# Performance work log

Hardware: AMD Instinct MI355X
Metric: run time of the kernel (lower is better)

The kernel has to match this reference:

```python
import jax, jax.numpy as jnp
import numpy as np

GRID_SIZE = 8
MARGIN = 1.0
NUM_NEG = 4
SOS_NEG = 8
LOSS_LAMBDA = 1.0
IMG_H, IMG_W = 960, 1280  # desc2 is the stride-GRID_SIZE feature map of this image
BIG = 5.0    # fill for radius-masked entries in FOS distance matrix (> max unit-desc dist 2)
HUGE = 1e6   # fill for invalid entries in SOS candidate scores


def _l2n(x, eps=1e-8):
    return x / (jnp.linalg.norm(x, axis=-1, keepdims=True) + eps)


def _pdist(a, b, eps=1e-12):
    # a: B x N x C, b: B x M x C -> B x N x M euclidean distances
    sq = (jnp.sum(a * a, -1)[..., :, None] + jnp.sum(b * b, -1)[..., None, :]
          - 2.0 * jnp.einsum('bnc,bmc->bnm', a, b))
    return jnp.sqrt(jnp.maximum(sq, eps))


def _bilinear(desc, pts):
    # desc: B x C x H x W, pts: B x N x 2 in (y, x) image-pixel coords -> B x N x C
    B, C, H, W = desc.shape
    g = pts / GRID_SIZE - 0.5  # image coords -> feature-grid coords
    gy = jnp.clip(g[..., 0], 0.0, H - 1.0)
    gx = jnp.clip(g[..., 1], 0.0, W - 1.0)
    y0 = jnp.clip(jnp.floor(gy).astype(jnp.int32), 0, H - 2)
    x0 = jnp.clip(jnp.floor(gx).astype(jnp.int32), 0, W - 2)
    wy = (gy - y0)[:, None, :]
    wx = (gx - x0)[:, None, :]
    flat = desc.reshape(B, C, H * W)
    gat = lambda yi, xi: jnp.take_along_axis(flat, (yi * W + xi)[:, None, :], axis=2)
    v00, v01 = gat(y0, x0), gat(y0, x0 + 1)
    v10, v11 = gat(y0 + 1, x0), gat(y0 + 1, x0 + 1)
    out = (v00 * (1 - wy) * (1 - wx) + v01 * (1 - wy) * wx
           + v10 * wy * (1 - wx) + v11 * wy * wx)
    return out.transpose(0, 2, 1)


def _forward(kp1, w_kp1, kp1_desc, desc2, homo12):
    r = 2.0 * GRID_SIZE  # spatial masking radius
    d1 = _l2n(kp1_desc)                       # B x N x C
    w_desc = _l2n(_bilinear(desc2, w_kp1))    # B x N x C interpolated warped descriptors

    # visibility of kp1 under homography homo12 (kp stored as (y, x))
    ones = jnp.ones_like(kp1[..., :1])
    p = jnp.concatenate([kp1[..., 1:2], kp1[..., 0:1], ones], -1)  # (x, y, 1)
    q = jnp.einsum('bij,bnj->bni', homo12, p)
    qx = q[..., 0] / (q[..., 2] + 1e-8)
    qy = q[..., 1] / (q[..., 2] + 1e-8)
    vis = ((qx >= 0) & (qx < IMG_W) & (qy >= 0) & (qy < IMG_H)).astype(d1.dtype)
    denom = jnp.sum(vis) + 1e-8

    # ---- FOS: hard quad triplet with radius masking ----
    pos = jnp.sqrt(jnp.sum((d1 - w_desc) ** 2, -1) + 1e-12)  # B x N
    D = _pdist(d1, w_desc)          # B x N x N cross descriptor distances
    s22 = _pdist(w_kp1, w_kp1)      # B x N x N warped-coordinate distances
    Dm = jnp.where(s22 <= r, BIG, D)  # mask spatial near-positives (incl. diagonal)
    neg1 = -jax.lax.top_k(-Dm, NUM_NEG)[0]                       # hardest negs per row anchor
    neg2 = -jax.lax.top_k(-Dm.transpose(0, 2, 1), NUM_NEG)[0]    # per column anchor
    t1 = jnp.mean(jax.nn.relu(MARGIN + pos[..., None] - neg1), -1)
    t2 = jnp.mean(jax.nn.relu(MARGIN + pos[..., None] - neg2), -1)
    fos = jnp.sum(vis * 0.5 * (t1 + t2)) / denom

    # ---- SOS: radius-masked second-order similarity regularizer ----
    s11 = _pdist(kp1, kp1)
    d11 = _pdist(d1, d1)
    d22 = _pdist(w_desc, w_desc)
    valid = (s11 > r) & (s22 > r)
    score = jnp.where(valid, d11, HUGE)
    nscore, idx = jax.lax.top_k(-score, SOS_NEG)  # sos_neg hardest valid neighbors
    sel_d11 = -nscore
    sel_d22 = jnp.take_along_axis(d22, idx, axis=2)
    diff2 = jnp.where(sel_d11 < HUGE * 0.1, (sel_d11 - sel_d22) ** 2, 0.0)
    sos_i = jnp.sqrt(jnp.sum(diff2, -1) + 1e-12)
    sos = jnp.sum(vis * sos_i) / denom

    return (fos + sos) * LOSS_LAMBDA


def setup_inputs() -> dict:
    key = jax.random.key(0)
    k1, k2, k3, k4, k5 = jax.random.split(key, 5)
    B, N, C, H, W = 2, 4096, 128, 120, 160
    scale = jnp.array([IMG_H - 1.0, IMG_W - 1.0], dtype=jnp.float32)
    kp1 = jax.random.uniform(k1, (B, N, 2), dtype=jnp.float32) * scale
    w_kp1 = jax.random.uniform(k2, (B, N, 2), dtype=jnp.float32) * scale
    kp1_desc = jax.random.normal(k3, (B, N, C), dtype=jnp.float32)
    desc2 = jax.random.normal(k4, (B, C, H, W), dtype=jnp.float32)
    homo12 = (jnp.tile(jnp.eye(3, dtype=jnp.float32), (B, 1, 1))
              + 0.001 * jax.random.normal(k5, (B, 3, 3), dtype=jnp.float32))
    return {'kp1': kp1, 'w_kp1': w_kp1, 'kp1_desc': kp1_desc,
            'desc2': desc2, 'homo12': homo12}


def reference(kp1, w_kp1, kp1_desc, desc2, homo12):
    return _forward(kp1, w_kp1, kp1_desc, desc2, homo12)
```

## Files before the change

### kernel.cpp

```cpp
#include <hip/hip_runtime.h>
#include <hip/hip_fp16.h>
#include <math.h>

#define NPTS 4096
#define CDIM 128
#define FH 120
#define FW 160
#define PIX (FH * FW)

typedef __attribute__((ext_vector_type(8))) short short8_t;
typedef __attribute__((ext_vector_type(4))) float float4_t;
typedef __attribute__((ext_vector_type(2))) unsigned short ushort2_t;

#define OFF_FRAG  0
#define OFF_WDB   1048576
#define OFF_JA    1572864
#define OFF_JB    1605632
#define OFF_POS   1622016
#define OFF_VIS   1630208
#define OFF_ACC   1638400
#define OFF_D2T   2031632
#define OFF_PARTS 2031632
#define OFF_END   4489232

__device__ __forceinline__ unsigned short f2bf(float f) {
  unsigned int u = __float_as_uint(f);
  u = (u + 0x7fffu + ((u >> 16) & 1u)) >> 16;
  return (unsigned short)u;
}

__device__ __forceinline__ float wavesum(float v) {
#pragma unroll
  for (int off = 1; off < 64; off <<= 1) v += __shfl_xor(v, off, 64);
  return v;
}

typedef const __attribute__((address_space(1))) unsigned int gu32_t;
typedef __attribute__((address_space(3))) unsigned int lu32_t;
__device__ __forceinline__ void gl_lds16(const void* g, void* l) {
  __builtin_amdgcn_global_load_lds((gu32_t*)g, (lu32_t*)l, 16, 0, 0);
}

__global__ __launch_bounds__(256) void transpose_desc2(
    const float* __restrict__ d2, unsigned short* __restrict__ out) {
  __shared__ unsigned short tile[64][130];
  const int bp = blockIdx.x;
  const int b = bp / 300;
  const int p0 = (bp - b * 300) * 64;
  const int tid = threadIdx.x;
  const int grp = tid >> 6, lp = tid & 63;
#pragma unroll 4
  for (int r = 0; r < 32; ++r) {
    int c = (r << 2) | grp;
    float v = d2[((size_t)b * CDIM + c) * PIX + p0 + lp];
    tile[lp][c] = __half_as_ushort(__float2half(v));
  }
  __syncthreads();
  unsigned int* ob = (unsigned int*)(out + ((size_t)b * PIX + p0) * CDIM);
#pragma unroll
  for (int i = 0; i < 16; ++i) {
    int u = (i << 8) | tid;
    int p = u >> 6, cc = (u & 63) << 1;
    unsigned int lo = tile[p][cc], hi = tile[p][cc + 1];
    ob[u] = lo | (hi << 16);
  }
}

#define PREP_TAIL() do {                                                        \
  {                                                                             \
    const int T = (p & (NPTS - 1)) >> 4, cRow = p & 15;                         \
    const int kcL = lane >> 4, quadL = (lane >> 2) & 3, jjL = (lane & 3) * 2;   \
    const size_t off = (size_t)(quadL * 16 + cRow) * 8 + jjL;                   \
    const size_t tb = (((size_t)b * 256 + T) * 2) * 4;                          \
    ushort2_t st; st.x = f2bf(d0); st.y = f2bf(d1v);                            \
    ushort2_t sw; sw.x = f2bf(e0); sw.y = f2bf(e1);                             \
    *(ushort2_t*)(frag + (tb + kcL) * 512 + off) = st;                          \
    *(ushort2_t*)(frag + (tb + 4 + kcL) * 512 + off) = sw;                      \
    ushort2_t swr; swr.x = f2bf(e0); swr.y = f2bf(e1);                          \
    *(ushort2_t*)(wdb + (size_t)p * CDIM + c2) = swr;                           \
  }                                                                             \
  float dd0 = d0 - e0, dd1 = d1v - e1;                                          \
  float ssp = wavesum(dd0 * dd0 + dd1 * dd1);                                   \
  if (lane == 0) {                                                              \
    pos[p] = sqrtf(ssp + 1e-12f);                                               \
    float ky = kp1[p * 2 + 0], kx = kp1[p * 2 + 1];                             \
    jA[p] = make_float4(ky, kx, y, x);                                          \
    jb1[p] = -0.5f * n1;                                                        \
    jb2[p] = -0.5f * n2;                                                        \
    const float* h = homo + b * 9;                                              \
    float t0 = h[0] * kx + h[1] * ky + h[2];                                    \
    float t1 = h[3] * kx + h[4] * ky + h[5];                                    \
    float t2 = h[6] * kx + h[7] * ky + h[8];                                    \
    float qx = t0 / (t2 + 1e-8f), qy = t1 / (t2 + 1e-8f);                       \
    vis[p] = (qx >= 0.0f && qx < 1280.0f && qy >= 0.0f && qy < 960.0f)          \
                 ? 1.0f : 0.0f;                                                 \
  }                                                                             \
} while (0)

__global__ __launch_bounds__(256) void prep_t(
    const float* __restrict__ kp1, const float* __restrict__ wkp1,
    const float* __restrict__ desc, const unsigned short* __restrict__ d2t,
    const float* __restrict__ homo,
    unsigned short* __restrict__ frag, unsigned short* __restrict__ wdb,
    float4* __restrict__ jA, float* __restrict__ jb1, float* __restrict__ jb2,
    float* __restrict__ pos, float* __restrict__ vis, float* __restrict__ acc) {
  const int tid = threadIdx.x;
  if (blockIdx.x == 0 && tid < 4) acc[tid] = 0.0f;
  const int p = blockIdx.x * 4 + (tid >> 6);
  const int lane = tid & 63;
  const int b = p >> 12;
  const int c2 = lane * 2;

  float2 v = *(const float2*)(desc + (size_t)p * CDIM + c2);
  float ss = wavesum(v.x * v.x + v.y * v.y);
  float inv = 1.0f / (sqrtf(ss) + 1e-8f);
  float d0 = v.x * inv, d1v = v.y * inv;
  float n1 = ss * inv * inv;

  float y = wkp1[p * 2 + 0], x = wkp1[p * 2 + 1];
  float gy = fminf(fmaxf(y * 0.125f - 0.5f, 0.0f), (float)(FH - 1));
  float gx = fminf(fmaxf(x * 0.125f - 0.5f, 0.0f), (float)(FW - 1));
  int y0 = (int)floorf(gy); y0 = min(max(y0, 0), FH - 2);
  int x0 = (int)floorf(gx); x0 = min(max(x0, 0), FW - 2);
  float wy = gy - (float)y0, wx = gx - (float)x0;
  float w00 = (1 - wy) * (1 - wx), w01 = (1 - wy) * wx;
  float w10 = wy * (1 - wx), w11 = wy * wx;
  const unsigned int* t00 = (const unsigned int*)
      (d2t + ((size_t)b * PIX + y0 * FW + x0) * CDIM) + lane;
  unsigned int u00 = t00[0], u01 = t00[64];
  unsigned int u10 = t00[FW * 64], u11 = t00[FW * 64 + 64];
  float2 f00 = __half22float2(*(const __half2*)&u00);
  float2 f01 = __half22float2(*(const __half2*)&u01);
  float2 f10 = __half22float2(*(const __half2*)&u10);
  float2 f11 = __half22float2(*(const __half2*)&u11);
  float wv0 = f00.x * w00 + f01.x * w01 + f10.x * w10 + f11.x * w11;
  float wv1 = f00.y * w00 + f01.y * w01 + f10.y * w10 + f11.y * w11;
  float ss2 = wavesum(wv0 * wv0 + wv1 * wv1);
  float inv2 = 1.0f / (sqrtf(ss2) + 1e-8f);
  float e0 = wv0 * inv2, e1 = wv1 * inv2;
  float n2 = ss2 * inv2 * inv2;

  PREP_TAIL();
}

__global__ __launch_bounds__(256) void prep_g(
    const float* __restrict__ kp1, const float* __restrict__ wkp1,
    const float* __restrict__ desc, const float* __restrict__ desc2,
    const float* __restrict__ homo,
    unsigned short* __restrict__ frag, unsigned short* __restrict__ wdb,
    float4* __restrict__ jA, float* __restrict__ jb1, float* __restrict__ jb2,
    float* __restrict__ pos, float* __restrict__ vis, float* __restrict__ acc) {
  const int tid = threadIdx.x;
  if (blockIdx.x == 0 && tid < 4) acc[tid] = 0.0f;
  const int p = blockIdx.x * 4 + (tid >> 6);
  const int lane = tid & 63;
  const int b = p >> 12;
  const int c2 = lane * 2;

  float2 v = *(const float2*)(desc + (size_t)p * CDIM + c2);
  float ss = wavesum(v.x * v.x + v.y * v.y);
  float inv = 1.0f / (sqrtf(ss) + 1e-8f);
  float d0 = v.x * inv, d1v = v.y * inv;
  float n1 = ss * inv * inv;

  float y = wkp1[p * 2 + 0], x = wkp1[p * 2 + 1];
  float gy = fminf(fmaxf(y * 0.125f - 0.5f, 0.0f), (float)(FH - 1));
  float gx = fminf(fmaxf(x * 0.125f - 0.5f, 0.0f), (float)(FW - 1));
  int y0 = (int)floorf(gy); y0 = min(max(y0, 0), FH - 2);
  int x0 = (int)floorf(gx); x0 = min(max(x0, 0), FW - 2);
  float wy = gy - (float)y0, wx = gx - (float)x0;
  float w00 = (1 - wy) * (1 - wx), w01 = (1 - wy) * wx;
  float w10 = wy * (1 - wx), w11 = wy * wx;
  const float* q0 = desc2 + ((size_t)b * CDIM + c2) * PIX + y0 * FW + x0;
  const float* q1 = q0 + PIX;
  float wv0 = q0[0] * w00 + q0[1] * w01 + q0[FW] * w10 + q0[FW + 1] * w11;
  float wv1 = q1[0] * w00 + q1[1] * w01 + q1[FW] * w10 + q1[FW + 1] * w11;
  float ss2 = wavesum(wv0 * wv0 + wv1 * wv1);
  float inv2 = 1.0f / (sqrtf(ss2) + 1e-8f);
  float e0 = wv0 * inv2, e1 = wv1 * inv2;
  float n2 = ss2 * inv2 * inv2;

  PREP_TAIL();
}

__device__ __forceinline__ void ins4m(float v, float* L) {
  float p0 = L[0]; L[0] = fmaxf(L[0], v);
  float p1 = L[1]; L[1] = __builtin_amdgcn_fmed3f(p0, L[1], v);
  float p2 = L[2]; L[2] = __builtin_amdgcn_fmed3f(p1, L[2], v);
  L[3] = __builtin_amdgcn_fmed3f(p2, L[3], v);
}
__device__ __forceinline__ void ins6m(float v, float* L) {
  float p0 = L[0]; L[0] = fmaxf(L[0], v);
  float p1 = L[1]; L[1] = __builtin_amdgcn_fmed3f(p0, L[1], v);
  float p2 = L[2]; L[2] = __builtin_amdgcn_fmed3f(p1, L[2], v);
  float p3 = L[3]; L[3] = __builtin_amdgcn_fmed3f(p2, L[3], v);
  float p4 = L[4]; L[4] = __builtin_amdgcn_fmed3f(p3, L[4], v);
  L[5] = __builtin_amdgcn_fmed3f(p4, L[5], v);
}
__device__ __forceinline__ void ins10m(float v, float* L) {
  float p0 = L[0]; L[0] = fmaxf(L[0], v);
  float pk = p0;
#pragma unroll
  for (int k = 1; k < 9; ++k) {
    float cur = L[k];
    L[k] = __builtin_amdgcn_fmed3f(pk, cur, v);
    pk = cur;
  }
  L[9] = __builtin_amdgcn_fmed3f(pk, L[9], v);
}

__device__ __forceinline__ float packkey(float s, int j) {
  return __uint_as_float((__float_as_uint(s) & 0xFFFFF000u) | (unsigned)j);
}

#define TILE_ONE(BP, J0, M1, M2) do {                                           \
  short8_t Ad[4], Aw[4];                                                        \
  _Pragma("unroll")                                                             \
  for (int kc = 0; kc < 4; ++kc) {                                              \
    Ad[kc] = *(const short8_t*)((BP) + kc * 512 + lane * 8);                    \
    Aw[kc] = *(const short8_t*)((BP) + (4 + kc) * 512 + lane * 8);              \
  }                                                                             \
  float4_t aD, aDt, a11;                                                        \
  aD[0] = (M2).x; aD[1] = (M2).y; aD[2] = (M2).z; aD[3] = (M2).w;               \
  aDt[0] = (M1).x; aDt[1] = (M1).y; aDt[2] = (M1).z; aDt[3] = (M1).w;           \
  a11 = aDt;                                                                    \
  __builtin_amdgcn_s_setprio(1);                                                \
  _Pragma("unroll")                                                             \
  for (int kc = 0; kc < 4; ++kc) {                                              \
    aD  = __builtin_amdgcn_mfma_f32_16x16x32_bf16(Aw[kc], Bd[kc], aD,  0,0,0);  \
    aDt = __builtin_amdgcn_mfma_f32_16x16x32_bf16(Ad[kc], Bw[kc], aDt, 0,0,0);  \
    a11 = __builtin_amdgcn_mfma_f32_16x16x32_bf16(Ad[kc], Bd[kc], a11, 0,0,0);  \
  }                                                                             \
  __builtin_amdgcn_s_setprio(0);                                                \
  _Pragma("unroll")                                                             \
  for (int reg = 0; reg < 4; ++reg) {                                           \
    const int jj = (J0) + (quad << 2) + reg;                                    \
    ins4m(packkey(aD[reg], jj), fD);                                            \
    ins4m(packkey(aDt[reg], jj), fDt);                                          \
    ins6m(packkey(a11[reg], jj), fS);                                           \
  }                                                                             \
} while (0)

#define STAGE_T(BI, TG) do {                                                    \
  gl_lds16((TG) + ch * 512 + lane * 8, &buf[BI][ch * 512]);                     \
  gl_lds16((TG) + (ch + 1) * 512 + lane * 8, &buf[BI][(ch + 1) * 512]);         \
} while (0)

__global__ __launch_bounds__(256, 4) void loss_main(
    const unsigned short* __restrict__ frag,
    const float* __restrict__ jb1g, const float* __restrict__ jb2g,
    float* __restrict__ parts) {
  __shared__ __align__(16) unsigned short buf[4][4096];

  const int tid = threadIdx.x;
  const int bid = blockIdx.x;
  const int combo = ((bid & 7) << 1) | (bid >> 9);
  const int b   = combo >> 3;
  const int seg = combo & 7;
  const int g   = (bid >> 3) & 63;
  const int wave = tid >> 6, lane = tid & 63;
  const int quad = lane >> 4;
  const int base = b * NPTS;
  const int jbase = seg << 9;

  short8_t Bd[4], Bw[4];
  {
    const unsigned short* fb =
        frag + (((size_t)b * 256 + (g * 4 + wave)) * 8) * 512 + (size_t)lane * 8;
#pragma unroll
    for (int kc = 0; kc < 4; ++kc) {
      Bd[kc] = *(const short8_t*)(fb + kc * 512);
      Bw[kc] = *(const short8_t*)(fb + (4 + kc) * 512);
    }
  }

  float fD[4], fDt[4], fS[6];
#pragma unroll
  for (int k = 0; k < 4; ++k) { fD[k] = -1e30f; fDt[k] = -1e30f; }
#pragma unroll
  for (int k = 0; k < 6; ++k) fS[k] = -1e30f;

  const unsigned short* fa = frag + (((size_t)b * 256 + (jbase >> 4)) * 8) * 512;
  const float* j1b = jb1g + base;
  const float* j2b = jb2g + base;
  const int ch = wave << 1;

  STAGE_T(0, fa);
  STAGE_T(1, fa + 4096);
  float4 m1c = *(const float4*)(j1b + jbase + (quad << 2));
  float4 m2c = *(const float4*)(j2b + jbase + (quad << 2));

  for (int t = 0; t < 30; ++t) {
    STAGE_T((t + 2) & 3, fa + (size_t)(t + 2) * 4096);
    const int jn = jbase + ((t + 1) << 4) + (quad << 2);
    float4 m1n = *(const float4*)(j1b + jn);
    float4 m2n = *(const float4*)(j2b + jn);
    asm volatile("s_waitcnt vmcnt(4)" ::: "memory");
    __builtin_amdgcn_s_barrier();
    asm volatile("" ::: "memory");
    TILE_ONE(&buf[t & 3][0], jbase + (t << 4), m1c, m2c);
    m1c = m1n; m2c = m2n;
  }
  {
    const int jn = jbase + (31 << 4) + (quad << 2);
    float4 m1n = *(const float4*)(j1b + jn);
    float4 m2n = *(const float4*)(j2b + jn);
    asm volatile("s_waitcnt vmcnt(2)" ::: "memory");
    __builtin_amdgcn_s_barrier();
    asm volatile("" ::: "memory");
    TILE_ONE(&buf[30 & 3][0], jbase + (30 << 4), m1c, m2c);
    m1c = m1n; m2c = m2n;
  }
  {
    asm volatile("s_waitcnt vmcnt(0)" ::: "memory");
    __builtin_amdgcn_s_barrier();
    asm volatile("" ::: "memory");
    TILE_ONE(&buf[31 & 3][0], jbase + (31 << 4), m1c, m2c);
  }

  float eD[6], eDt[6], eS[10];
#pragma unroll
  for (int k = 0; k < 4; ++k) { eD[k] = fD[k]; eDt[k] = fDt[k]; }
  eD[4] = eD[5] = eDt[4] = eDt[5] = -1e30f;
#pragma unroll
  for (int k = 0; k < 6; ++k) eS[k] = fS[k];
  eS[6] = eS[7] = eS[8] = eS[9] = -1e30f;

  {
    float tmp[10];
#pragma unroll
    for (int off = 16; off <= 32; off <<= 1) {
#pragma unroll
      for (int k = 0; k < 6; ++k) tmp[k] = eD[k];
#pragma unroll
      for (int k = 0; k < 6; ++k) ins6m(__shfl_xor(tmp[k], off, 64), eD);
#pragma unroll
      for (int k = 0; k < 6; ++k) tmp[k] = eDt[k];
#pragma unroll
      for (int k = 0; k < 6; ++k) ins6m(__shfl_xor(tmp[k], off, 64), eDt);
#pragma unroll
      for (int k = 0; k < 10; ++k) tmp[k] = eS[k];
#pragma unroll
      for (int k = 0; k < 10; ++k) ins10m(__shfl_xor(tmp[k], off, 64), eS);
    }
  }

  if (lane < 16) {
    float* P = parts + (size_t)(seg * 22) * 8192 +
               (base + g * 64 + wave * 16 + lane);
#pragma unroll
    for (int k = 0; k < 6; ++k) {
      P[(size_t)k * 8192] = eD[k];
      P[(size_t)(6 + k) * 8192] = eDt[k];
    }
#pragma unroll
    for (int k = 0; k < 10; ++k) P[(size_t)(12 + k) * 8192] = eS[k];
  }
}

__device__ __forceinline__ float bflo(unsigned int u) { return __uint_as_float(u << 16); }
__device__ __forceinline__ float bfhi(unsigned int u) { return __uint_as_float(u & 0xFFFF0000u); }

__global__ __launch_bounds__(256) void merge_filter(
    const float* __restrict__ parts, const float4* __restrict__ jAg,
    const float* __restrict__ jb1g, const float* __restrict__ jb2g,
    const float* __restrict__ posg,
    const float* __restrict__ visg, const unsigned short* __restrict__ wdb,
    float* __restrict__ accum, float* __restrict__ out) {
  __shared__ int sJ[256];
  __shared__ float sD11[256], sD22[256], sT[64], sVis[32], sN2[32];
  const int tid = threadIdx.x;
  const int a0 = blockIdx.x * 32;

  if (tid < 64) {
    const int al = tid & 31;
    const int type = tid >> 5;
    const int a = a0 + al;
    const int base = a & ~(NPTS - 1);
    float L[6];
#pragma unroll
    for (int k = 0; k < 6; ++k) L[k] = -1e30f;
    const float* P = parts + (size_t)(type * 6) * 8192 + a;
#pragma unroll
    for (int s = 0; s < 8; ++s) {
#pragma unroll
      for (int k = 0; k < 6; ++k) ins6m(P[(size_t)(s * 22 + k) * 8192], L);
    }
    const float4 own = jAg[a];
    const float pv = posg[a];
    const float nsel = -2.0f * (type ? jb2g[a] : jb1g[a]);
    float ts = 0.0f;
    int got = 0;
#pragma unroll
    for (int k = 0; k < 6; ++k) {
      int j = (int)(__float_as_uint(L[k]) & 0xFFFu);
      float4 jc = jAg[base + j];
      float dz = own.z - jc.z, dw = own.w - jc.w;
      if (got < 4 && dz * dz + dw * dw > 256.0f) {
        float d2 = fmaf(-2.0f, L[k], nsel);
        ts += fmaxf(1.0f + pv - sqrtf(fmaxf(d2, 1e-12f)), 0.0f);
        got++;
      }
    }
    sT[tid] = ts;
  } else if (tid < 96) {
    const int al = tid - 64;
    const int a = a0 + al;
    const int base = a & ~(NPTS - 1);
    float S[10];
#pragma unroll
    for (int k = 0; k < 10; ++k) S[k] = -1e30f;
    const float* P = parts + (size_t)12 * 8192 + a;
#pragma unroll
    for (int s = 0; s < 8; ++s) {
#pragma unroll
      for (int k = 0; k < 10; ++k) ins10m(P[(size_t)(s * 22 + k) * 8192], S);
    }
    const float4 own = jAg[a];
    const float n1i = -2.0f * jb1g[a];
    int m = 0;
#pragma unroll
    for (int k = 0; k < 10; ++k) {
      int j = (int)(__float_as_uint(S[k]) & 0xFFFu);
      float4 jc = jAg[base + j];
      float ay = own.x - jc.x, ax = own.y - jc.y;
      float wz = own.z - jc.z, ww = own.w - jc.w;
      if (m < 8 && ay * ay + ax * ax > 256.0f && wz * wz + ww * ww > 256.0f) {
        sJ[al * 8 + m] = base + j;
        sD11[al * 8 + m] = sqrtf(fmaxf(fmaf(-2.0f, S[k], n1i), 1e-12f));
        m++;
      }
    }
    for (int k = m; k < 8; ++k) sJ[al * 8 + k] = -1;
    sVis[al] = visg[a];
    sN2[al] = -2.0f * jb2g[a];
  }
  __syncthreads();

  {
    const int slot = tid;
    const int al = slot >> 3;
    const int j = sJ[slot];
    float d22 = 0.0f;
    if (j >= 0) {
      const uint4* pi = (const uint4*)(wdb + (size_t)(a0 + al) * CDIM);
      const uint4* pj = (const uint4*)(wdb + (size_t)j * CDIM);
      float dot = 0.0f;
#pragma unroll
      for (int qq = 0; qq < 16; ++qq) {
        uint4 ui = pi[qq], uj = pj[qq];
        dot = fmaf(bflo(ui.x), bflo(uj.x), dot); dot = fmaf(bfhi(ui.x), bfhi(uj.x), dot);
        dot = fmaf(bflo(ui.y), bflo(uj.y), dot); dot = fmaf(bfhi(ui.y), bfhi(uj.y), dot);
        dot = fmaf(bflo(ui.z), bflo(uj.z), dot); dot = fmaf(bfhi(ui.z), bfhi(uj.z), dot);
        dot = fmaf(bflo(ui.w), bflo(uj.w), dot); dot = fmaf(bfhi(ui.w), bfhi(uj.w), dot);
      }
      d22 = sqrtf(fmaxf(fmaf(-2.0f, jb2g[j] + dot, sN2[al]), 1e-12f));
    }
    sD22[slot] = d22;
  }
  __syncthreads();

  float contrib = 0.0f, vsum = 0.0f;
  if (tid < 32) {
    float s = 0.0f;
#pragma unroll
    for (int k = 0; k < 8; ++k) {
      if (sJ[tid * 8 + k] >= 0) {
        float d = sD11[tid * 8 + k] - sD22[tid * 8 + k];
        s = fmaf(d, d, s);
      }
    }
    contrib = sVis[tid] * (0.125f * (sT[tid] + sT[32 + tid]) + sqrtf(s + 1e-12f));
    vsum = sVis[tid];
  }
  if (tid < 64) {
#pragma unroll
    for (int off = 32; off >= 1; off >>= 1) {
      contrib += __shfl_down(contrib, off, 64);
      vsum += __shfl_down(vsum, off, 64);
    }
    if (tid == 0) {
      atomicAdd(&accum[0], contrib);
      atomicAdd(&accum[1], vsum);
      __threadfence();
      float old = atomicAdd(&accum[2], 1.0f);
      if (old == 255.0f) {
        float t = atomicAdd(&accum[0], 0.0f);
        float v = atomicAdd(&accum[1], 0.0f);
        out[0] = t / (v + 1e-8f);
      }
    }
  }
}

extern "C" void kernel_launch(void* const* d_in, const int* in_sizes, int n_in,
                              void* d_out, int out_size, void* d_ws, size_t ws_size,
                              hipStream_t stream) {
  (void)in_sizes; (void)n_in; (void)out_size;
  const float* kp1   = (const float*)d_in[0];
  const float* wkp1  = (const float*)d_in[1];
  const float* desc  = (const float*)d_in[2];
  const float* desc2 = (const float*)d_in[3];
  const float* homo  = (const float*)d_in[4];
  float* ws = (float*)d_ws;
  unsigned short* frag = (unsigned short*)(ws + OFF_FRAG);
  unsigned short* wdb  = (unsigned short*)(ws + OFF_WDB);
  float4* jA = (float4*)(ws + OFF_JA);
  float* jb1 = ws + OFF_JB;
  float* jb2 = ws + OFF_JB + 8192;
  float* pos = ws + OFF_POS;
  float* vis = ws + OFF_VIS;
  float* acc = ws + OFF_ACC;
  float* parts = ws + OFF_PARTS;
  unsigned short* d2t = (unsigned short*)(ws + OFF_D2T);

  if (ws_size >= (size_t)OFF_END * 4) {
    transpose_desc2<<<600, 256, 0, stream>>>(desc2, d2t);
    prep_t<<<2048, 256, 0, stream>>>(kp1, wkp1, desc, d2t, homo,
                                     frag, wdb, jA, jb1, jb2, pos, vis, acc);
  } else {
    prep_g<<<2048, 256, 0, stream>>>(kp1, wkp1, desc, desc2, homo,
                                     frag, wdb, jA, jb1, jb2, pos, vis, acc);
  }
  loss_main<<<1024, 256, 0, stream>>>(frag, jb1, jb2, parts);
  merge_filter<<<256, 256, 0, stream>>>(parts, jA, jb1, jb2, pos, vis, wdb, acc,
                                        (float*)d_out);
}
```

Baseline: 149.6 us.

## Switch pairwise distance kernel to 32x32x16 MFMA tiles with larger chunks

Reorganizes the bf16 fragment layout into 32-point tiles and moves the main all-pairs kernel from 16x16x32 to 32x32x16 MFMA, so each wave holds a 32-row B fragment and processes 32-column chunks staged through a 4-deep LDS pipeline. The jb norms are preloaded into LDS, the grid is halved to 512 blocks with lower occupancy, and top-k per lane widens (6/6/8 instead of 4/4/6) with only one cross-half shuffle merge. The aim is fewer MFMA issues, fewer reloads of the A chunks and a cheaper reduction, at the cost of more registers, larger partial-result buffers and more insertion work in merge_filter.

```diff
diff --git a/kernel.cpp b/kernel.cpp
--- a/kernel.cpp
+++ b/kernel.cpp
@@ -10,6 +10,7 @@
 
 typedef __attribute__((ext_vector_type(8))) short short8_t;
 typedef __attribute__((ext_vector_type(4))) float float4_t;
+typedef __attribute__((ext_vector_type(16))) float f32x16_t;
 typedef __attribute__((ext_vector_type(2))) unsigned short ushort2_t;
 
 #define OFF_FRAG  0
@@ -68,14 +69,15 @@
 
 #define PREP_TAIL() do {                                                        \
   {                                                                             \
-    const int T = (p & (NPTS - 1)) >> 4, cRow = p & 15;                         \
-    const int kcL = lane >> 4, quadL = (lane >> 2) & 3, jjL = (lane & 3) * 2;   \
-    const size_t off = (size_t)(quadL * 16 + cRow) * 8 + jjL;                   \
-    const size_t tb = (((size_t)b * 256 + T) * 2) * 4;                          \
+    const int pc = p & (NPTS - 1);                                              \
+    const int Tc = pc >> 5, m = pc & 31;                                        \
+    const int kq = lane >> 3, hi2 = (lane >> 2) & 1, j0 = (lane & 3) * 2;       \
+    const size_t off = (size_t)kq * 512 + (m + 32 * hi2) * 8 + j0;              \
+    const size_t cb = ((size_t)b * 128 + Tc) * 8192;                            \
     ushort2_t st; st.x = f2bf(d0); st.y = f2bf(d1v);                            \
     ushort2_t sw; sw.x = f2bf(e0); sw.y = f2bf(e1);                             \
-    *(ushort2_t*)(frag + (tb + kcL) * 512 + off) = st;                          \
-    *(ushort2_t*)(frag + (tb + 4 + kcL) * 512 + off) = sw;                      \
+    *(ushort2_t*)(frag + cb + off) = st;                                        \
+    *(ushort2_t*)(frag + cb + 4096 + off) = sw;                                 \
     ushort2_t swr; swr.x = f2bf(e0); swr.y = f2bf(e1);                          \
     *(ushort2_t*)(wdb + (size_t)p * CDIM + c2) = swr;                           \
   }                                                                             \
@@ -183,12 +185,6 @@
   PREP_TAIL();
 }
 
-__device__ __forceinline__ void ins4m(float v, float* L) {
-  float p0 = L[0]; L[0] = fmaxf(L[0], v);
-  float p1 = L[1]; L[1] = __builtin_amdgcn_fmed3f(p0, L[1], v);
-  float p2 = L[2]; L[2] = __builtin_amdgcn_fmed3f(p1, L[2], v);
-  L[3] = __builtin_amdgcn_fmed3f(p2, L[3], v);
-}
 __device__ __forceinline__ void ins6m(float v, float* L) {
   float p0 = L[0]; L[0] = fmaxf(L[0], v);
   float p1 = L[1]; L[1] = __builtin_amdgcn_fmed3f(p0, L[1], v);
@@ -197,164 +193,172 @@
   float p4 = L[4]; L[4] = __builtin_amdgcn_fmed3f(p3, L[4], v);
   L[5] = __builtin_amdgcn_fmed3f(p4, L[5], v);
 }
-__device__ __forceinline__ void ins10m(float v, float* L) {
+__device__ __forceinline__ void ins8m(float v, float* L) {
   float p0 = L[0]; L[0] = fmaxf(L[0], v);
   float pk = p0;
 #pragma unroll
-  for (int k = 1; k < 9; ++k) {
+  for (int k = 1; k < 7; ++k) {
     float cur = L[k];
     L[k] = __builtin_amdgcn_fmed3f(pk, cur, v);
     pk = cur;
   }
-  L[9] = __builtin_amdgcn_fmed3f(pk, L[9], v);
+  L[7] = __builtin_amdgcn_fmed3f(pk, L[7], v);
+}
+__device__ __forceinline__ void ins12m(float v, float* L) {
+  float p0 = L[0]; L[0] = fmaxf(L[0], v);
+  float pk = p0;
+#pragma unroll
+  for (int k = 1; k < 11; ++k) {
+    float cur = L[k];
+    L[k] = __builtin_amdgcn_fmed3f(pk, cur, v);
+    pk = cur;
+  }
+  L[11] = __builtin_amdgcn_fmed3f(pk, L[11], v);
 }
 
 __device__ __forceinline__ float packkey(float s, int j) {
   return __uint_as_float((__float_as_uint(s) & 0xFFFFF000u) | (unsigned)j);
 }
 
-#define TILE_ONE(BP, J0, M1, M2) do {                                           \
-  short8_t Ad[4], Aw[4];                                                        \
+#define CHUNK(T) do {                                                           \
+  const unsigned short* bp = &buf[(T) & 3][0];                                  \
+  float4 m1v[4], m2v[4];                                                        \
   _Pragma("unroll")                                                             \
-  for (int kc = 0; kc < 4; ++kc) {                                              \
-    Ad[kc] = *(const short8_t*)((BP) + kc * 512 + lane * 8);                    \
-    Aw[kc] = *(const short8_t*)((BP) + (4 + kc) * 512 + lane * 8);              \
+  for (int q = 0; q < 4; ++q) {                                                 \
+    m1v[q] = *(const float4*)&jbL[(T) * 32 + q * 8 + hi * 4];                   \
+    m2v[q] = *(const float4*)&jbL[512 + (T) * 32 + q * 8 + hi * 4];             \
   }                                                                             \
-  float4_t aD, aDt, a11;                                                        \
-  aD[0] = (M2).x; aD[1] = (M2).y; aD[2] = (M2).z; aD[3] = (M2).w;               \
-  aDt[0] = (M1).x; aDt[1] = (M1).y; aDt[2] = (M1).z; aDt[3] = (M1).w;           \
-  a11 = aDt;                                                                    \
+  f32x16_t aD, aDt, a11;                                                        \
+  _Pragma("unroll")                                                             \
+  for (int q = 0; q < 4; ++q) {                                                 \
+    _Pragma("unroll")                                                           \
+    for (int i = 0; i < 4; ++i) {                                               \
+      aD[q * 4 + i] = m2v[q][i];                                                \
+      aDt[q * 4 + i] = m1v[q][i];                                               \
+      a11[q * 4 + i] = m1v[q][i];                                               \
+    }                                                                           \
+  }                                                                             \
   __builtin_amdgcn_s_setprio(1);                                                \
   _Pragma("unroll")                                                             \
-  for (int kc = 0; kc < 4; ++kc) {                                              \
-    aD  = __builtin_amdgcn_mfma_f32_16x16x32_bf16(Aw[kc], Bd[kc], aD,  0,0,0);  \
-    aDt = __builtin_amdgcn_mfma_f32_16x16x32_bf16(Ad[kc], Bw[kc], aDt, 0,0,0);  \
-    a11 = __builtin_amdgcn_mfma_f32_16x16x32_bf16(Ad[kc], Bd[kc], a11, 0,0,0);  \
+  for (int kq = 0; kq < 8; ++kq) {                                              \
+    short8_t Ad = *(const short8_t*)(bp + kq * 512 + lane * 8);                 \
+    short8_t Aw = *(const short8_t*)(bp + 4096 + kq * 512 + lane * 8);          \
+    aD  = __builtin_amdgcn_mfma_f32_32x32x16_bf16(Aw, Bd[kq], aD,  0, 0, 0);    \
+    aDt = __builtin_amdgcn_mfma_f32_32x32x16_bf16(Ad, Bw[kq], aDt, 0, 0, 0);    \
+    a11 = __builtin_amdgcn_mfma_f32_32x32x16_bf16(Ad, Bd[kq], a11, 0, 0, 0);    \
   }                                                                             \
   __builtin_amdgcn_s_setprio(0);                                                \
+  const int jjp = jbase + (T) * 32 + (hi << 2);                                 \
   _Pragma("unroll")                                                             \
-  for (int reg = 0; reg < 4; ++reg) {                                           \
-    const int jj = (J0) + (quad << 2) + reg;                                    \
-    ins4m(packkey(aD[reg], jj), fD);                                            \
-    ins4m(packkey(aDt[reg], jj), fDt);                                          \
-    ins6m(packkey(a11[reg], jj), fS);                                           \
+  for (int reg = 0; reg < 16; ++reg) {                                          \
+    const int jj = jjp | ((reg & 3) | ((reg >> 2) << 3));                       \
+    ins6m(packkey(aD[reg], jj), fD);                                            \
+    ins6m(packkey(aDt[reg], jj), fDt);                                          \
+    ins8m(packkey(a11[reg], jj), fS);                                           \
   }                                                                             \
 } while (0)
 
-#define STAGE_T(BI, TG) do {                                                    \
-  gl_lds16((TG) + ch * 512 + lane * 8, &buf[BI][ch * 512]);                     \
-  gl_lds16((TG) + (ch + 1) * 512 + lane * 8, &buf[BI][(ch + 1) * 512]);         \
+#define STAGE_C(BI, CT) do {                                                    \
+  const unsigned short* gsrc =                                                  \
+      fa + (size_t)(CT) * 8192 + wave * 512 + lane * 8;                         \
+  _Pragma("unroll")                                                             \
+  for (int i = 0; i < 4; ++i)                                                   \
+    gl_lds16(gsrc + i * 2048, &buf[BI][i * 2048 + wave * 512]);                 \
 } while (0)
 
-__global__ __launch_bounds__(256, 4) void loss_main(
+__global__ __launch_bounds__(256, 2) void loss_main(
     const unsigned short* __restrict__ frag,
     const float* __restrict__ jb1g, const float* __restrict__ jb2g,
     float* __restrict__ parts) {
-  __shared__ __align__(16) unsigned short buf[4][4096];
+  __shared__ __align__(16) unsigned short buf[4][8192];
+  __shared__ __align__(16) float jbL[1024];
 
   const int tid = threadIdx.x;
   const int bid = blockIdx.x;
-  const int combo = ((bid & 7) << 1) | (bid >> 9);
+  const int combo = ((bid & 7) << 1) | (bid >> 8);
   const int b   = combo >> 3;
   const int seg = combo & 7;
-  const int g   = (bid >> 3) & 63;
+  const int g   = (bid >> 3) & 31;
   const int wave = tid >> 6, lane = tid & 63;
-  const int quad = lane >> 4;
+  const int hi = lane >> 5;
   const int base = b * NPTS;
   const int jbase = seg << 9;
 
-  short8_t Bd[4], Bw[4];
+  short8_t Bd[8], Bw[8];
   {
     const unsigned short* fb =
-        frag + (((size_t)b * 256 + (g * 4 + wave)) * 8) * 512 + (size_t)lane * 8;
-#pragma unroll
-    for (int kc = 0; kc < 4; ++kc) {
-      Bd[kc] = *(const short8_t*)(fb + kc * 512);
-      Bw[kc] = *(const short8_t*)(fb + (4 + kc) * 512);
-    }
-  }
-
-  float fD[4], fDt[4], fS[6];
-#pragma unroll
-  for (int k = 0; k < 4; ++k) { fD[k] = -1e30f; fDt[k] = -1e30f; }
-#pragma unroll
-  for (int k = 0; k < 6; ++k) fS[k] = -1e30f;
-
-  const unsigned short* fa = frag + (((size_t)b * 256 + (jbase >> 4)) * 8) * 512;
-  const float* j1b = jb1g + base;
-  const float* j2b = jb2g + base;
-  const int ch = wave << 1;
-
-  STAGE_T(0, fa);
-  STAGE_T(1, fa + 4096);
-  float4 m1c = *(const float4*)(j1b + jbase + (quad << 2));
-  float4 m2c = *(const float4*)(j2b + jbase + (quad << 2));
-
-  for (int t = 0; t < 30; ++t) {
-    STAGE_T((t + 2) & 3, fa + (size_t)(t + 2) * 4096);
-    const int jn = jbase + ((t + 1) << 4) + (quad << 2);
-    float4 m1n = *(const float4*)(j1b + jn);
-    float4 m2n = *(const float4*)(j2b + jn);
-    asm volatile("s_waitcnt vmcnt(4)" ::: "memory");
+        frag + ((size_t)b * 128 + (g * 4 + wave)) * 8192 + (size_t)lane * 8;
+#pragma unroll
+    for (int kq = 0; kq < 8; ++kq) {
+      Bd[kq] = *(const short8_t*)(fb + kq * 512);
+      Bw[kq] = *(const short8_t*)(fb + 4096 + kq * 512);
+    }
+  }
+
+  if (wave == 0) {
+    gl_lds16(jb1g + base + jbase + lane * 4, &jbL[0]);
+    gl_lds16(jb1g + base + jbase + 256 + lane * 4, &jbL[256]);
+  } else if (wave == 1) {
+    gl_lds16(jb2g + base + jbase + lane * 4, &jbL[512]);
+    gl_lds16(jb2g + base + jbase + 256 + lane * 4, &jbL[768]);
+  }
+
+  float fD[6], fDt[6], fS[8];
+#pragma unroll
+  for (int k = 0; k < 6; ++k) { fD[k] = -1e30f; fDt[k] = -1e30f; }
+#pragma unroll
+  for (int k = 0; k < 8; ++k) fS[k] = -1e30f;
+
+  const unsigned short* fa = frag + ((size_t)b * 128 + (jbase >> 5)) * 8192;
+
+  STAGE_C(0, 0);
+  STAGE_C(1, 1);
+  STAGE_C(2, 2);
+  asm volatile("s_waitcnt vmcnt(8)" ::: "memory");
+  __builtin_amdgcn_s_barrier();
+  asm volatile("" ::: "memory");
+
+  for (int t = 0; t < 13; ++t) {
+    STAGE_C((t + 3) & 3, t + 3);
+    CHUNK(t);
+    asm volatile("s_waitcnt vmcnt(8)" ::: "memory");
     __builtin_amdgcn_s_barrier();
     asm volatile("" ::: "memory");
-    TILE_ONE(&buf[t & 3][0], jbase + (t << 4), m1c, m2c);
-    m1c = m1n; m2c = m2n;
-  }
-  {
-    const int jn = jbase + (31 << 4) + (quad << 2);
-    float4 m1n = *(const float4*)(j1b + jn);
-    float4 m2n = *(const float4*)(j2b + jn);
-    asm volatile("s_waitcnt vmcnt(2)" ::: "memory");
-    __builtin_amdgcn_s_barrier();
-    asm volatile("" ::: "memory");
-    TILE_ONE(&buf[30 & 3][0], jbase + (30 << 4), m1c, m2c);
-    m1c = m1n; m2c = m2n;
-  }
-  {
-    asm volatile("s_waitcnt vmcnt(0)" ::: "memory");
-    __builtin_amdgcn_s_barrier();
-    asm volatile("" ::: "memory");
-    TILE_ONE(&buf[31 & 3][0], jbase + (31 << 4), m1c, m2c);
-  }
-
-  float eD[6], eDt[6], eS[10];
-#pragma unroll
-  for (int k = 0; k < 4; ++k) { eD[k] = fD[k]; eDt[k] = fDt[k]; }
-  eD[4] = eD[5] = eDt[4] = eDt[5] = -1e30f;
-#pragma unroll
-  for (int k = 0; k < 6; ++k) eS[k] = fS[k];
-  eS[6] = eS[7] = eS[8] = eS[9] = -1e30f;
-
-  {
-    float tmp[10];
-#pragma unroll
-    for (int off = 16; off <= 32; off <<= 1) {
-#pragma unroll
-      for (int k = 0; k < 6; ++k) tmp[k] = eD[k];
-#pragma unroll
-      for (int k = 0; k < 6; ++k) ins6m(__shfl_xor(tmp[k], off, 64), eD);
-#pragma unroll
-      for (int k = 0; k < 6; ++k) tmp[k] = eDt[k];
-#pragma unroll
-      for (int k = 0; k < 6; ++k) ins6m(__shfl_xor(tmp[k], off, 64), eDt);
-#pragma unroll
-      for (int k = 0; k < 10; ++k) tmp[k] = eS[k];
-#pragma unroll
-      for (int k = 0; k < 10; ++k) ins10m(__shfl_xor(tmp[k], off, 64), eS);
-    }
-  }
-
-  if (lane < 16) {
-    float* P = parts + (size_t)(seg * 22) * 8192 +
-               (base + g * 64 + wave * 16 + lane);
-#pragma unroll
-    for (int k = 0; k < 6; ++k) {
+  }
+  CHUNK(13);
+  asm volatile("s_waitcnt vmcnt(4)" ::: "memory");
+  __builtin_amdgcn_s_barrier();
+  asm volatile("" ::: "memory");
+  CHUNK(14);
+  asm volatile("s_waitcnt vmcnt(0)" ::: "memory");
+  __builtin_amdgcn_s_barrier();
+  asm volatile("" ::: "memory");
+  CHUNK(15);
+
+  float eD[8], eDt[8], eS[12];
+#pragma unroll
+  for (int k = 0; k < 6; ++k) { eD[k] = fD[k]; eDt[k] = fDt[k]; }
+  eD[6] = eD[7] = eDt[6] = eDt[7] = -1e30f;
+#pragma unroll
+  for (int k = 0; k < 8; ++k) eS[k] = fS[k];
+  eS[8] = eS[9] = eS[10] = eS[11] = -1e30f;
+#pragma unroll
+  for (int k = 0; k < 6; ++k) ins8m(__shfl_xor(fD[k], 32, 64), eD);
+#pragma unroll
+  for (int k = 0; k < 6; ++k) ins8m(__shfl_xor(fDt[k], 32, 64), eDt);
+#pragma unroll
+  for (int k = 0; k < 8; ++k) ins12m(__shfl_xor(fS[k], 32, 64), eS);
+
+  if (lane < 32) {
+    float* P = parts + (size_t)(seg * 28) * 8192 +
+               (base + g * 128 + wave * 32 + lane);
+#pragma unroll
+    for (int k = 0; k < 8; ++k) {
       P[(size_t)k * 8192] = eD[k];
-      P[(size_t)(6 + k) * 8192] = eDt[k];
-    }
-#pragma unroll
-    for (int k = 0; k < 10; ++k) P[(size_t)(12 + k) * 8192] = eS[k];
+      P[(size_t)(8 + k) * 8192] = eDt[k];
+    }
+#pragma unroll
+    for (int k = 0; k < 12; ++k) P[(size_t)(16 + k) * 8192] = eS[k];
   }
 }
 
@@ -377,14 +381,14 @@
     const int type = tid >> 5;
     const int a = a0 + al;
     const int base = a & ~(NPTS - 1);
-    float L[6];
-#pragma unroll
-    for (int k = 0; k < 6; ++k) L[k] = -1e30f;
-    const float* P = parts + (size_t)(type * 6) * 8192 + a;
+    float L[8];
+#pragma unroll
+    for (int k = 0; k < 8; ++k) L[k] = -1e30f;
+    const float* P = parts + (size_t)(type * 8) * 8192 + a;
 #pragma unroll
     for (int s = 0; s < 8; ++s) {
 #pragma unroll
-      for (int k = 0; k < 6; ++k) ins6m(P[(size_t)(s * 22 + k) * 8192], L);
+      for (int k = 0; k < 8; ++k) ins8m(P[(size_t)(s * 28 + k) * 8192], L);
     }
     const float4 own = jAg[a];
     const float pv = posg[a];
@@ -392,7 +396,7 @@
     float ts = 0.0f;
     int got = 0;
 #pragma unroll
-    for (int k = 0; k < 6; ++k) {
+    for (int k = 0; k < 8; ++k) {
       int j = (int)(__float_as_uint(L[k]) & 0xFFFu);
       float4 jc = jAg[base + j];
       float dz = own.z - jc.z, dw = own.w - jc.w;
@@ -407,20 +411,20 @@
     const int al = tid - 64;
     const int a = a0 + al;
     const int base = a & ~(NPTS - 1);
-    float S[10];
-#pragma unroll
-    for (int k = 0; k < 10; ++k) S[k] = -1e30f;
-    const float* P = parts + (size_t)12 * 8192 + a;
+    float S[12];
+#pragma unroll
+    for (int k = 0; k < 12; ++k) S[k] = -1e30f;
+    const float* P = parts + a;
 #pragma unroll
     for (int s = 0; s < 8; ++s) {
 #pragma unroll
-      for (int k = 0; k < 10; ++k) ins10m(P[(size_t)(s * 22 + k) * 8192], S);
+      for (int k = 0; k < 12; ++k) ins12m(P[(size_t)(s * 28 + 16 + k) * 8192], S);
     }
     const float4 own = jAg[a];
     const float n1i = -2.0f * jb1g[a];
     int m = 0;
 #pragma unroll
-    for (int k = 0; k < 10; ++k) {
+    for (int k = 0; k < 12; ++k) {
       int j = (int)(__float_as_uint(S[k]) & 0xFFFu);
       float4 jc = jAg[base + j];
       float ay = own.x - jc.x, ax = own.y - jc.y;
@@ -522,7 +526,7 @@
     prep_g<<<2048, 256, 0, stream>>>(kp1, wkp1, desc, desc2, homo,
                                      frag, wdb, jA, jb1, jb2, pos, vis, acc);
   }
-  loss_main<<<1024, 256, 0, stream>>>(frag, jb1, jb2, parts);
+  loss_main<<<512, 256, 0, stream>>>(frag, jb1, jb2, parts);
   merge_filter<<<256, 256, 0, stream>>>(parts, jA, jb1, jb2, pos, vis, wdb, acc,
                                         (float*)d_out);
 }
```

After: 152.0 us. About the same (+1.7%).
